# Kernel optimization log

Measured on AMD Instinct MI355X. Metric: run time of the kernel, lower is better.

Reference implementation:

```python
import jax, jax.numpy as jnp
import numpy as np

B, S, I = 16, 512, 64
D, H, L, F = 512, 8, 6, 2048
MAX_REL = 32
EPS = 1e-5


def setup_inputs() -> dict:
    key = jax.random.key(0)
    ks = jax.random.split(key, 16)
    sc = 0.02
    inp = {
        "x": jax.random.normal(ks[0], (B, S, I), dtype=jnp.float32),
        "in_W": jax.random.normal(ks[1], (I, D), dtype=jnp.float32) * sc,
        "in_b": jnp.zeros((D,), jnp.float32),
        "rel_emb": jax.random.normal(ks[2], (2 * MAX_REL + 1, D), dtype=jnp.float32) * sc,
        "qkvo_W": jax.random.normal(ks[3], (L, 4, D, D), dtype=jnp.float32) * sc,
        "qkvo_b": jnp.zeros((L, 4, D), jnp.float32),
        "ln_g": jnp.ones((L, 2, D), jnp.float32),
        "ln_b": jnp.zeros((L, 2, D), jnp.float32),
        "ff_W1": jax.random.normal(ks[4], (L, D, F), dtype=jnp.float32) * sc,
        "ff_b1": jnp.zeros((L, F), jnp.float32),
        "ff_W2": jax.random.normal(ks[5], (L, F, D), dtype=jnp.float32) * sc,
        "ff_b2": jnp.zeros((L, D), jnp.float32),
        "out_W": jax.random.normal(ks[6], (D, 1), dtype=jnp.float32) * sc,
        "out_b": jnp.zeros((1,), jnp.float32),
    }
    return inp


def _layernorm(x, g, b):
    mu = jnp.mean(x, axis=-1, keepdims=True)
    var = jnp.mean((x - mu) ** 2, axis=-1, keepdims=True)
    return (x - mu) * jax.lax.rsqrt(var + EPS) * g + b


def reference(x, in_W, in_b, rel_emb, qkvo_W, qkvo_b, ln_g, ln_b, ff_W1, ff_b1, ff_W2, ff_b2, out_W, out_b):
    b, s, _ = x.shape
    dk = D // H
    h = x @ in_W + in_b  # (B,S,D)
    # relative positional encoding: mean over query axis of gathered embeddings
    pos = jnp.arange(s)
    rel = jnp.clip(pos[:, None] - pos[None, :], -MAX_REL, MAX_REL) + MAX_REL  # (S,S)
    rp = rel_emb[rel]  # (S,S,D)
    h = h + rp.mean(axis=0)[None]  # broadcast over batch

    def layer(h, p):
        Wqkvo, bqkvo, g, bl, W1, b1, W2, b2 = p
        def proj(i):
            return (h @ Wqkvo[i] + bqkvo[i]).reshape(b, s, H, dk).transpose(0, 2, 1, 3)
        q, k, v = proj(0), proj(1), proj(2)  # (B,H,S,dk)
        scores = jnp.einsum("bhqd,bhkd->bhqk", q, k) / jnp.sqrt(jnp.float32(dk))
        attn = jax.nn.softmax(scores, axis=-1)
        ctx = jnp.einsum("bhqk,bhkd->bhqd", attn, v)
        ctx = ctx.transpose(0, 2, 1, 3).reshape(b, s, D)
        ao = ctx @ Wqkvo[3] + bqkvo[3]
        h1 = _layernorm(h + ao, g[0], bl[0])
        ff = jax.nn.relu(h1 @ W1 + b1) @ W2 + b2
        h2 = _layernorm(h1 + ff, g[1], bl[1])
        return h2, None

    h, _ = jax.lax.scan(layer, h, (qkvo_W, qkvo_b, ln_g, ln_b, ff_W1, ff_b1, ff_W2, ff_b2))
    out = h @ out_W + out_b  # (B,S,1)
    return out
```

## Files before the change

kernel.cpp:

```cpp
#include <hip/hip_runtime.h>
#include <math.h>

#define B 16
#define S 512
#define IN 64
#define D 512
#define H 8
#define DK 64
#define L 6
#define F 2048
#define BS (B*S)
#define EPS 1e-5f

typedef short short8 __attribute__((ext_vector_type(8)));
typedef short short4v __attribute__((ext_vector_type(4)));
typedef float floatx4 __attribute__((ext_vector_type(4)));

static __device__ inline short f2bf(float x) {
    unsigned u = __float_as_uint(x);
    unsigned r = (u + 0x7fffu + ((u >> 16) & 1u)) >> 16;
    return (short)r;
}
static __device__ inline float bf2f(short s) {
    return __uint_as_float(((unsigned)(unsigned short)s) << 16);
}

__global__ __launch_bounds__(256) void pe_kernel(const float* __restrict__ rel_emb,
                                                 float* __restrict__ pe) {
    int k = blockIdx.x;
    int d = threadIdx.x;
    float acc0 = 0.f, acc1 = 0.f;
    for (int r = 0; r < 65; ++r) {
        float w;
        if (r == 0)       w = (float)max(0, k - 31);
        else if (r == 64) w = (float)max(0, S - (k + 32));
        else {
            int qpos = k + r - 32;
            w = (qpos >= 0 && qpos < S) ? 1.f : 0.f;
        }
        acc0 += w * rel_emb[r * D + d];
        acc1 += w * rel_emb[r * D + d + 256];
    }
    pe[k * D + d]       = acc0 * (1.f / (float)S);
    pe[k * D + d + 256] = acc1 * (1.f / (float)S);
}

__global__ __launch_bounds__(256) void wtrans_kernel(const float* __restrict__ src,
                                                     short* __restrict__ dst,
                                                     int K, int N) {
    __shared__ float Ls[32][33];
    const int z = blockIdx.z, kb = blockIdx.y, nb = blockIdx.x;
    const int tx = threadIdx.x & 31, ty = threadIdx.x >> 5;
    src += (size_t)z * K * N;
    dst += (size_t)z * K * N;
#pragma unroll
    for (int i = 0; i < 4; ++i)
        Ls[ty + i * 8][tx] = src[(size_t)(kb * 32 + ty + i * 8) * N + nb * 32 + tx];
    __syncthreads();
#pragma unroll
    for (int i = 0; i < 4; ++i) {
        int n = nb * 32 + ty + i * 8;
        dst[(size_t)n * K + kb * 32 + tx] = f2bf(Ls[tx][ty + i * 8]);
    }
}

__global__ __launch_bounds__(256) void cvt_kernel(const float* __restrict__ in,
                                                  short* __restrict__ out) {
    int i = (blockIdx.x * 256 + threadIdx.x) * 4;
    float4 v = *(const float4*)(in + i);
    short4v o;
    o.x = f2bf(v.x); o.y = f2bf(v.y); o.z = f2bf(v.z); o.w = f2bf(v.w);
    *(short4v*)(out + i) = o;
}

__global__ __launch_bounds__(256) void vtrans_kernel(const short* __restrict__ v,
                                                     short* __restrict__ vt) {
    __shared__ short Ls[64 * 72];
    const int bh = blockIdx.y, jt = blockIdx.x * 64;
    const int t = threadIdx.x;
    const int r = t >> 2, cg = t & 3;
    *(short8*)&Ls[r * 72 + cg * 8] =
        *(const short8*)(v + ((size_t)bh * S + jt + r) * DK + cg * 8);
    *(short8*)&Ls[r * 72 + 32 + cg * 8] =
        *(const short8*)(v + ((size_t)bh * S + jt + r) * DK + 32 + cg * 8);
    __syncthreads();
    const int d = t >> 2, sg = t & 3;
    short tmp[16];
#pragma unroll
    for (int i = 0; i < 16; ++i) tmp[i] = Ls[(sg * 16 + i) * 72 + d];
    short* dst = vt + ((size_t)bh * DK + d) * S + jt + sg * 16;
    *(short8*)(dst)     = *(short8*)&tmp[0];
    *(short8*)(dst + 8) = *(short8*)&tmp[8];
}

#define GLL(SRC, DST) __builtin_amdgcn_global_load_lds( \
    (const __attribute__((address_space(1))) void*)(SRC), \
    (__attribute__((address_space(3))) void*)(DST), 16, 0, 0)

#define SWAIT4 __builtin_amdgcn_s_waitcnt(0x0F74)
#define SWAIT0 __builtin_amdgcn_s_waitcnt(0x0F70)

#define KITER(CUR_A, CUR_B, NXT_A, NXT_B, I)                              \
  {                                                                       \
    if ((I) + 1 < niter) SWAIT4; else SWAIT0;                             \
    __builtin_amdgcn_s_barrier();                                         \
    const int kn_ = ((I) + 2) << 5;                                       \
    if (kn_ < K) {                                                        \
      GLL(Ag0 + kn_, NXT_A + so0); GLL(Ag1 + kn_, NXT_A + so1);           \
      GLL(Bg0 + kn_, NXT_B + so0); GLL(Bg1 + kn_, NXT_B + so1);           \
    }                                                                     \
    short8 af_[4], bf_[4];                                                \
    _Pragma("unroll")                                                     \
    for (int mt = 0; mt < 4; ++mt) {                                      \
      af_[mt] = *(const short8*)&CUR_A[((wm * 4 + mt) * 64 + slot) * 8];  \
      bf_[mt] = *(const short8*)&CUR_B[((wn * 4 + mt) * 64 + slot) * 8];  \
    }                                                                     \
    _Pragma("unroll")                                                     \
    for (int mt = 0; mt < 4; ++mt)                                        \
      _Pragma("unroll")                                                   \
      for (int nt = 0; nt < 4; ++nt)                                      \
        acc[mt][nt] = __builtin_amdgcn_mfma_f32_16x16x32_bf16(            \
            af_[mt], bf_[nt], acc[mt][nt], 0, 0, 0);                      \
  }

__global__ __launch_bounds__(256) void mfma_gemm(
    const short* __restrict__ A, const short* __restrict__ Bt,
    const float* __restrict__ bias, short* __restrict__ Cb,
    float* __restrict__ Cf, int M, int N, int K, int lda, int ldb, int mode,
    const float* __restrict__ pe, long az, long wz, long bz, long cz)
{
    __shared__ short As0[4096], As1[4096], As2[4096];
    __shared__ short Bs0[4096], Bs1[4096], Bs2[4096];

    const int z = blockIdx.z;
    const short* Az = A  + (size_t)z * az;
    const short* Bz = Bt + (size_t)z * wz;

    const int t = threadIdx.x;
    const int w = t >> 6, lane = t & 63;
    const int wm = w >> 1, wn = w & 1;
    const int ln15 = lane & 15, lq = lane >> 4;
    const int bm = blockIdx.y, bn = blockIdx.x;

    const int ml = lane >> 2;
    const int kb = ((lane & 3) - (ml >> 1)) & 3;
    const short* Ag0 = Az + (size_t)(bm * 128 + w * 16 + ml)       * lda + kb * 8;
    const short* Ag1 = Az + (size_t)(bm * 128 + (w + 4) * 16 + ml) * lda + kb * 8;
    const short* Bg0 = Bz + (size_t)(bn * 128 + w * 16 + ml)       * ldb + kb * 8;
    const short* Bg1 = Bz + (size_t)(bn * 128 + (w + 4) * 16 + ml) * ldb + kb * 8;
    const int so0 = w * 512, so1 = (w + 4) * 512;

    floatx4 acc[4][4] = {};
    const int slot = ln15 * 4 + ((lq + (ln15 >> 1)) & 3);
    const int niter = K >> 5;

    GLL(Ag0, As0 + so0); GLL(Ag1, As0 + so1);
    GLL(Bg0, Bs0 + so0); GLL(Bg1, Bs0 + so1);
    if (niter > 1) {
        GLL(Ag0 + 32, As1 + so0); GLL(Ag1 + 32, As1 + so1);
        GLL(Bg0 + 32, Bs1 + so0); GLL(Bg1 + 32, Bs1 + so1);
    }

    int i = 0;
    for (; i + 3 <= niter; i += 3) {
        KITER(As0, Bs0, As2, Bs2, i);
        KITER(As1, Bs1, As0, Bs0, i + 1);
        KITER(As2, Bs2, As1, Bs1, i + 2);
    }
    if (i < niter)     KITER(As0, Bs0, As2, Bs2, i);
    if (i + 1 < niter) KITER(As1, Bs1, As0, Bs0, i + 1);

    short* Cbz = Cb + (size_t)z * cz;
    float* Cfz = Cf + (size_t)z * cz;
    const float* bb = bias + (size_t)z * bz;
#pragma unroll
    for (int mt = 0; mt < 4; ++mt) {
#pragma unroll
        for (int nt = 0; nt < 4; ++nt) {
            const int col = bn * 128 + wn * 64 + nt * 16 + ln15;
            const int row0 = bm * 128 + wm * 64 + mt * 16 + lq * 4;
            const float bc = (mode == 4) ? 0.f : bb[col];
#pragma unroll
            for (int reg = 0; reg < 4; ++reg) {
                const int r = row0 + reg;
                float v = acc[mt][nt][reg] + bc;
                if (mode == 4) {
                    Cfz[(size_t)r * N + col] = v;
                } else if (mode == 3) {
                    const int bi = r >> 9, si = r & (S - 1);
                    const int hh = col >> 6, dd = col & 63;
                    Cbz[(((size_t)(bi * H + hh) * S + si) * DK + dd)] = f2bf(v);
                } else {
                    if (mode == 1) v = fmaxf(v, 0.f);
                    else if (mode == 2) v += pe[(size_t)(r & (S - 1)) * D + col];
                    Cb[(size_t)r * N + col] = f2bf(v);
                }
            }
        }
    }
}

__global__ __launch_bounds__(256) void attn_mfma(
    const short* __restrict__ qg, const short* __restrict__ kg,
    const short* __restrict__ vtg, short* __restrict__ ctx)
{
    __shared__ short Ks[64 * 72];
    __shared__ short Vs[64 * 72];
    __shared__ short Ps[4][16 * 72];

    const int t = threadIdx.x;
    const int w = t >> 6, lane = t & 63;
    const int ln15 = lane & 15, lq = lane >> 4;
    const int bh = blockIdx.y, bi = bh >> 3, hh = bh & 7;
    const int qbase = blockIdx.x * 64 + w * 16;

    short8 qf0, qf1;
    {
        const short* qrow = qg + ((size_t)bh * S + qbase + ln15) * DK;
        qf0 = *(const short8*)(qrow + lq * 8);
        qf1 = *(const short8*)(qrow + 32 + lq * 8);
    }
    floatx4 o[4] = {};
    float mrow[4] = {-1e30f, -1e30f, -1e30f, -1e30f};
    float lrow[4] = {};

    const int sr = t >> 2, scg = t & 3;
    const short* kbase = kg  + (size_t)bh * S * DK;
    const short* vtb   = vtg + (size_t)bh * DK * S;

    for (int jt = 0; jt < S; jt += 64) {
        __syncthreads();
        *(short8*)&Ks[sr * 72 + scg * 8] =
            *(const short8*)(kbase + (size_t)(jt + sr) * DK + scg * 8);
        *(short8*)&Ks[sr * 72 + 32 + scg * 8] =
            *(const short8*)(kbase + (size_t)(jt + sr) * DK + 32 + scg * 8);
        *(short8*)&Vs[sr * 72 + scg * 8] =
            *(const short8*)(vtb + (size_t)sr * S + jt + scg * 8);
        *(short8*)&Vs[sr * 72 + 32 + scg * 8] =
            *(const short8*)(vtb + (size_t)sr * S + jt + 32 + scg * 8);
        __syncthreads();

        floatx4 sc[4];
#pragma unroll
        for (int nt = 0; nt < 4; ++nt) {
            floatx4 s4 = {};
            short8 kf0 = *(const short8*)&Ks[(nt * 16 + ln15) * 72 + lq * 8];
            short8 kf1 = *(const short8*)&Ks[(nt * 16 + ln15) * 72 + 32 + lq * 8];
            s4 = __builtin_amdgcn_mfma_f32_16x16x32_bf16(qf0, kf0, s4, 0, 0, 0);
            s4 = __builtin_amdgcn_mfma_f32_16x16x32_bf16(qf1, kf1, s4, 0, 0, 0);
#pragma unroll
            for (int r = 0; r < 4; ++r) s4[r] *= 0.125f;
            sc[nt] = s4;
        }

        float rmax[4];
#pragma unroll
        for (int r = 0; r < 4; ++r)
            rmax[r] = fmaxf(fmaxf(sc[0][r], sc[1][r]), fmaxf(sc[2][r], sc[3][r]));
#pragma unroll
        for (int off = 1; off < 16; off <<= 1)
#pragma unroll
            for (int r = 0; r < 4; ++r)
                rmax[r] = fmaxf(rmax[r], __shfl_xor(rmax[r], off));

        float mnew[4], alpha[4], psum[4];
#pragma unroll
        for (int r = 0; r < 4; ++r) {
            mnew[r]  = fmaxf(mrow[r], rmax[r]);
            alpha[r] = __expf(mrow[r] - mnew[r]);
            psum[r]  = 0.f;
        }
#pragma unroll
        for (int nt = 0; nt < 4; ++nt)
#pragma unroll
            for (int r = 0; r < 4; ++r) {
                float p = __expf(sc[nt][r] - mnew[r]);
                psum[r] += p;
                Ps[w][(lq * 4 + r) * 72 + nt * 16 + ln15] = f2bf(p);
            }
#pragma unroll
        for (int off = 1; off < 16; off <<= 1)
#pragma unroll
            for (int r = 0; r < 4; ++r)
                psum[r] += __shfl_xor(psum[r], off);
#pragma unroll
        for (int r = 0; r < 4; ++r) {
            lrow[r] = lrow[r] * alpha[r] + psum[r];
            mrow[r] = mnew[r];
        }
#pragma unroll
        for (int dv = 0; dv < 4; ++dv)
#pragma unroll
            for (int r = 0; r < 4; ++r)
                o[dv][r] *= alpha[r];

        short8 pf0 = *(const short8*)&Ps[w][ln15 * 72 + lq * 8];
        short8 pf1 = *(const short8*)&Ps[w][ln15 * 72 + 32 + lq * 8];
#pragma unroll
        for (int dv = 0; dv < 4; ++dv) {
            short8 vf0 = *(const short8*)&Vs[(dv * 16 + ln15) * 72 + lq * 8];
            short8 vf1 = *(const short8*)&Vs[(dv * 16 + ln15) * 72 + 32 + lq * 8];
            o[dv] = __builtin_amdgcn_mfma_f32_16x16x32_bf16(pf0, vf0, o[dv], 0, 0, 0);
            o[dv] = __builtin_amdgcn_mfma_f32_16x16x32_bf16(pf1, vf1, o[dv], 0, 0, 0);
        }
    }

    float inv[4];
#pragma unroll
    for (int r = 0; r < 4; ++r) inv[r] = 1.f / lrow[r];
#pragma unroll
    for (int dv = 0; dv < 4; ++dv)
#pragma unroll
        for (int r = 0; r < 4; ++r) {
            const int s = qbase + lq * 4 + r;
            const int col = hh * DK + dv * 16 + ln15;
            ctx[((size_t)bi * S + s) * D + col] = f2bf(o[dv][r] * inv[r]);
        }
}

__global__ __launch_bounds__(128) void ln_res_kernel(
    const short* __restrict__ a, const float* __restrict__ p0,
    const float* __restrict__ p1, const float* __restrict__ eb,
    const float* __restrict__ g, const float* __restrict__ beta,
    short* __restrict__ outb)
{
    const int row = blockIdx.x;
    const int t = threadIdx.x;
    const size_t off = (size_t)row * D + t * 4;
    const short4v xa = *(const short4v*)(a + off);
    const float4 q0 = *(const float4*)(p0 + off);
    const float4 q1 = *(const float4*)(p1 + off);
    const float4 bb2 = *(const float4*)(eb + t * 4);
    float x0 = bf2f(xa.x) + q0.x + q1.x + bb2.x;
    float x1 = bf2f(xa.y) + q0.y + q1.y + bb2.y;
    float x2 = bf2f(xa.z) + q0.z + q1.z + bb2.z;
    float x3 = bf2f(xa.w) + q0.w + q1.w + bb2.w;
    float s  = x0 + x1 + x2 + x3;
    float s2 = x0 * x0 + x1 * x1 + x2 * x2 + x3 * x3;
#pragma unroll
    for (int o = 32; o > 0; o >>= 1) {
        s  += __shfl_down(s, o);
        s2 += __shfl_down(s2, o);
    }
    __shared__ float red[2][2];
    const int wave = t >> 6;
    if ((t & 63) == 0) { red[wave][0] = s; red[wave][1] = s2; }
    __syncthreads();
    s  = red[0][0] + red[1][0];
    s2 = red[0][1] + red[1][1];
    const float mu  = s * (1.f / (float)D);
    const float var = s2 * (1.f / (float)D) - mu * mu;
    const float r   = rsqrtf(var + EPS);
    const float4 gg = *(const float4*)(g    + t * 4);
    const float4 bb = *(const float4*)(beta + t * 4);
    short4v ob;
    ob.x = f2bf((x0 - mu) * r * gg.x + bb.x);
    ob.y = f2bf((x1 - mu) * r * gg.y + bb.y);
    ob.z = f2bf((x2 - mu) * r * gg.z + bb.z);
    ob.w = f2bf((x3 - mu) * r * gg.w + bb.w);
    *(short4v*)(outb + off) = ob;
}

__global__ __launch_bounds__(256) void out_kernel(
    const short* __restrict__ h, const float* __restrict__ ow,
    const float* __restrict__ ob, float* __restrict__ out)
{
    const int wave = threadIdx.x >> 6;
    const int lane = threadIdx.x & 63;
    const int row  = blockIdx.x * 4 + wave;
    const short* hp = h + (size_t)row * D;
    float s = 0.f;
#pragma unroll
    for (int u = 0; u < 8; ++u) {
        int d = lane + u * 64;
        s += bf2f(hp[d]) * ow[d];
    }
#pragma unroll
    for (int o = 32; o > 0; o >>= 1) s += __shfl_down(s, o);
    if (lane == 0) out[row] = s + ob[0];
}

extern "C" void kernel_launch(void* const* d_in, const int* in_sizes, int n_in,
                              void* d_out, int out_size, void* d_ws, size_t ws_size,
                              hipStream_t stream) {
    const float* x       = (const float*)d_in[0];
    const float* in_W    = (const float*)d_in[1];
    const float* in_b    = (const float*)d_in[2];
    const float* rel_emb = (const float*)d_in[3];
    const float* qkvo_W  = (const float*)d_in[4];
    const float* qkvo_b  = (const float*)d_in[5];
    const float* ln_g    = (const float*)d_in[6];
    const float* ln_bb   = (const float*)d_in[7];
    const float* ff_W1   = (const float*)d_in[8];
    const float* ff_b1   = (const float*)d_in[9];
    const float* ff_W2   = (const float*)d_in[10];
    const float* ff_b2   = (const float*)d_in[11];
    const float* out_W   = (const float*)d_in[12];
    const float* out_b   = (const float*)d_in[13];
    float* out = (float*)d_out;

    const size_t HSZ = (size_t)BS * D;
    float* pe     = (float*)d_ws;
    float* part0  = pe + (size_t)S * D;
    float* part1  = part0 + HSZ;
    short* h_bf   = (short*)(part1 + HSZ);
    short* h1_bf  = h_bf  + HSZ;
    short* qkv_bf = h1_bf + HSZ;
    short* xb     = qkv_bf + 4 * HSZ;
    short* wt_qkvo = xb + (size_t)BS * IN;
    short* wt_ff1  = wt_qkvo + (size_t)L * 4 * D * D;
    short* wt_ff2  = wt_ff1  + (size_t)L * D * F;
    short* wt_in   = wt_ff2  + (size_t)L * F * D;

    const size_t CZ = (size_t)B * H * S * DK;
    short* qb = qkv_bf;
    short* kb = qkv_bf + CZ;
    short* vb = qkv_bf + 2 * CZ;
    short* vt = qkv_bf + 3 * CZ;
    short* ctx_bf = vb;
    short* ff1_bf = qkv_bf;

    dim3 blk(256);

    pe_kernel<<<dim3(S), blk, 0, stream>>>(rel_emb, pe);
    cvt_kernel<<<dim3(BS * IN / 1024), blk, 0, stream>>>(x, xb);
    wtrans_kernel<<<dim3(D / 32, IN / 32, 1), blk, 0, stream>>>(in_W, wt_in, IN, D);
    wtrans_kernel<<<dim3(D / 32, D / 32, 4 * L), blk, 0, stream>>>(qkvo_W, wt_qkvo, D, D);
    wtrans_kernel<<<dim3(F / 32, D / 32, L), blk, 0, stream>>>(ff_W1, wt_ff1, D, F);
    wtrans_kernel<<<dim3(D / 32, F / 32, L), blk, 0, stream>>>(ff_W2, wt_ff2, F, D);

    mfma_gemm<<<dim3(D / 128, BS / 128, 1), blk, 0, stream>>>(
        xb, wt_in, in_b, h_bf, nullptr, BS, D, IN, IN, IN, 2, pe, 0, 0, 0, 0);

    for (int l = 0; l < L; ++l) {
        const float* bl = qkvo_b + (size_t)l * 4 * D;
        mfma_gemm<<<dim3(D / 128, BS / 128, 3), blk, 0, stream>>>(
            h_bf, wt_qkvo + (size_t)l * 4 * D * D, bl, qkv_bf, nullptr,
            BS, D, D, D, D, 3, nullptr, 0, (long)D * D, (long)D, (long)CZ);
        vtrans_kernel<<<dim3(S / 64, B * H), blk, 0, stream>>>(vb, vt);
        attn_mfma<<<dim3(S / 64, B * H), blk, 0, stream>>>(qb, kb, vt, ctx_bf);
        mfma_gemm<<<dim3(D / 128, BS / 128, 2), blk, 0, stream>>>(
            ctx_bf, wt_qkvo + (size_t)(l * 4 + 3) * D * D, nullptr, nullptr, part0,
            BS, D, 256, D, D, 4, nullptr, 256, 256, 0, (long)HSZ);
        ln_res_kernel<<<dim3(BS), dim3(128), 0, stream>>>(
            h_bf, part0, part1, bl + 3 * D,
            ln_g + (size_t)l * 2 * D, ln_bb + (size_t)l * 2 * D, h1_bf);
        mfma_gemm<<<dim3(F / 128, BS / 128, 1), blk, 0, stream>>>(
            h1_bf, wt_ff1 + (size_t)l * D * F, ff_b1 + (size_t)l * F, ff1_bf, nullptr,
            BS, F, D, D, D, 1, nullptr, 0, 0, 0, 0);
        mfma_gemm<<<dim3(D / 128, BS / 128, 2), blk, 0, stream>>>(
            ff1_bf, wt_ff2 + (size_t)l * F * D, nullptr, nullptr, part0,
            BS, D, 1024, F, F, 4, nullptr, 1024, 1024, 0, (long)HSZ);
        ln_res_kernel<<<dim3(BS), dim3(128), 0, stream>>>(
            h1_bf, part0, part1, ff_b2 + (size_t)l * D,
            ln_g + (size_t)l * 2 * D + D, ln_bb + (size_t)l * 2 * D + D, h_bf);
    }

    out_kernel<<<dim3(BS / 4), blk, 0, stream>>>(h_bf, out_W, out_b, out);
}
```

Baseline: 1.267 ms.

## Replace split-K fp32 partials with 128x64 tile GEMM and fuse V transpose

Two narrow N=512 GEMMs used split-K over two z-slices writing fp32 partials that layernorm then summed. They now use a new 128x64-tile kernel over the full K, adding bias and writing bf16 output directly. This doubles the block count without split-K and cuts fp32 partial traffic. The V projection is written transposed straight from the QKV GEMM epilogue, removing the separate vtrans kernel. The cost is strided scattered stores for V and rounding the residual branch to bf16 before layernorm.

After: 1.206 ms. 1.05x faster.

```diff
diff --git a/kernel.cpp b/kernel.cpp
--- a/kernel.cpp
+++ b/kernel.cpp
@@ -73,31 +73,12 @@
     *(short4v*)(out + i) = o;
 }
 
-__global__ __launch_bounds__(256) void vtrans_kernel(const short* __restrict__ v,
-                                                     short* __restrict__ vt) {
-    __shared__ short Ls[64 * 72];
-    const int bh = blockIdx.y, jt = blockIdx.x * 64;
-    const int t = threadIdx.x;
-    const int r = t >> 2, cg = t & 3;
-    *(short8*)&Ls[r * 72 + cg * 8] =
-        *(const short8*)(v + ((size_t)bh * S + jt + r) * DK + cg * 8);
-    *(short8*)&Ls[r * 72 + 32 + cg * 8] =
-        *(const short8*)(v + ((size_t)bh * S + jt + r) * DK + 32 + cg * 8);
-    __syncthreads();
-    const int d = t >> 2, sg = t & 3;
-    short tmp[16];
-#pragma unroll
-    for (int i = 0; i < 16; ++i) tmp[i] = Ls[(sg * 16 + i) * 72 + d];
-    short* dst = vt + ((size_t)bh * DK + d) * S + jt + sg * 16;
-    *(short8*)(dst)     = *(short8*)&tmp[0];
-    *(short8*)(dst + 8) = *(short8*)&tmp[8];
-}
-
 #define GLL(SRC, DST) __builtin_amdgcn_global_load_lds( \
     (const __attribute__((address_space(1))) void*)(SRC), \
     (__attribute__((address_space(3))) void*)(DST), 16, 0, 0)
 
 #define SWAIT4 __builtin_amdgcn_s_waitcnt(0x0F74)
+#define SWAIT3 __builtin_amdgcn_s_waitcnt(0x0F73)
 #define SWAIT0 __builtin_amdgcn_s_waitcnt(0x0F70)
 
 #define KITER(CUR_A, CUR_B, NXT_A, NXT_B, I)                              \
@@ -126,14 +107,13 @@
 __global__ __launch_bounds__(256) void mfma_gemm(
     const short* __restrict__ A, const short* __restrict__ Bt,
     const float* __restrict__ bias, short* __restrict__ Cb,
-    float* __restrict__ Cf, int M, int N, int K, int lda, int ldb, int mode,
-    const float* __restrict__ pe, long az, long wz, long bz, long cz)
+    int M, int N, int K, int lda, int ldb, int mode,
+    const float* __restrict__ pe, long wz, long bz, long cz)
 {
     __shared__ short As0[4096], As1[4096], As2[4096];
     __shared__ short Bs0[4096], Bs1[4096], Bs2[4096];
 
     const int z = blockIdx.z;
-    const short* Az = A  + (size_t)z * az;
     const short* Bz = Bt + (size_t)z * wz;
 
     const int t = threadIdx.x;
@@ -144,8 +124,8 @@
 
     const int ml = lane >> 2;
     const int kb = ((lane & 3) - (ml >> 1)) & 3;
-    const short* Ag0 = Az + (size_t)(bm * 128 + w * 16 + ml)       * lda + kb * 8;
-    const short* Ag1 = Az + (size_t)(bm * 128 + (w + 4) * 16 + ml) * lda + kb * 8;
+    const short* Ag0 = A  + (size_t)(bm * 128 + w * 16 + ml)       * lda + kb * 8;
+    const short* Ag1 = A  + (size_t)(bm * 128 + (w + 4) * 16 + ml) * lda + kb * 8;
     const short* Bg0 = Bz + (size_t)(bn * 128 + w * 16 + ml)       * ldb + kb * 8;
     const short* Bg1 = Bz + (size_t)(bn * 128 + (w + 4) * 16 + ml) * ldb + kb * 8;
     const int so0 = w * 512, so1 = (w + 4) * 512;
@@ -171,7 +151,6 @@
     if (i + 1 < niter) KITER(As1, Bs1, As0, Bs0, i + 1);
 
     short* Cbz = Cb + (size_t)z * cz;
-    float* Cfz = Cf + (size_t)z * cz;
     const float* bb = bias + (size_t)z * bz;
 #pragma unroll
     for (int mt = 0; mt < 4; ++mt) {
@@ -179,22 +158,102 @@
         for (int nt = 0; nt < 4; ++nt) {
             const int col = bn * 128 + wn * 64 + nt * 16 + ln15;
             const int row0 = bm * 128 + wm * 64 + mt * 16 + lq * 4;
-            const float bc = (mode == 4) ? 0.f : bb[col];
+            const float bc = bb[col];
 #pragma unroll
             for (int reg = 0; reg < 4; ++reg) {
                 const int r = row0 + reg;
                 float v = acc[mt][nt][reg] + bc;
-                if (mode == 4) {
-                    Cfz[(size_t)r * N + col] = v;
-                } else if (mode == 3) {
+                if (mode == 3) {
                     const int bi = r >> 9, si = r & (S - 1);
                     const int hh = col >> 6, dd = col & 63;
-                    Cbz[(((size_t)(bi * H + hh) * S + si) * DK + dd)] = f2bf(v);
+                    if (z == 2)
+                        Cbz[(((size_t)(bi * H + hh) * DK + dd) * S + si)] = f2bf(v);
+                    else
+                        Cbz[(((size_t)(bi * H + hh) * S + si) * DK + dd)] = f2bf(v);
                 } else {
                     if (mode == 1) v = fmaxf(v, 0.f);
                     else if (mode == 2) v += pe[(size_t)(r & (S - 1)) * D + col];
                     Cb[(size_t)r * N + col] = f2bf(v);
                 }
+            }
+        }
+    }
+}
+
+#define KITER64(CUR_A, CUR_B, NXT_A, NXT_B, I)                            \
+  {                                                                       \
+    if ((I) + 1 < niter) SWAIT3; else SWAIT0;                             \
+    __builtin_amdgcn_s_barrier();                                         \
+    const int kn_ = ((I) + 2) << 5;                                       \
+    if (kn_ < K) {                                                        \
+      GLL(Ag0 + kn_, NXT_A + so0); GLL(Ag1 + kn_, NXT_A + so1);           \
+      GLL(Bg0 + kn_, NXT_B + sob);                                        \
+    }                                                                     \
+    short8 af_[2], bf_[4];                                                \
+    _Pragma("unroll")                                                     \
+    for (int mt = 0; mt < 2; ++mt)                                        \
+      af_[mt] = *(const short8*)&CUR_A[((w * 2 + mt) * 64 + slot) * 8];   \
+    _Pragma("unroll")                                                     \
+    for (int nt = 0; nt < 4; ++nt)                                        \
+      bf_[nt] = *(const short8*)&CUR_B[(nt * 64 + slot) * 8];             \
+    _Pragma("unroll")                                                     \
+    for (int mt = 0; mt < 2; ++mt)                                        \
+      _Pragma("unroll")                                                   \
+      for (int nt = 0; nt < 4; ++nt)                                      \
+        acc[mt][nt] = __builtin_amdgcn_mfma_f32_16x16x32_bf16(            \
+            af_[mt], bf_[nt], acc[mt][nt], 0, 0, 0);                      \
+  }
+
+__global__ __launch_bounds__(256) void mfma_gemm_n64(
+    const short* __restrict__ A, const short* __restrict__ Bt,
+    const float* __restrict__ bias, short* __restrict__ Cb,
+    int M, int N, int K, int lda, int ldb, int mode)
+{
+    __shared__ short As0[4096], As1[4096], As2[4096];
+    __shared__ short Bs0[2048], Bs1[2048], Bs2[2048];
+
+    const int t = threadIdx.x;
+    const int w = t >> 6, lane = t & 63;
+    const int ln15 = lane & 15, lq = lane >> 4;
+    const int bm = blockIdx.y, bn = blockIdx.x;
+
+    const int ml = lane >> 2;
+    const int kb = ((lane & 3) - (ml >> 1)) & 3;
+    const short* Ag0 = A  + (size_t)(bm * 128 + w * 16 + ml)       * lda + kb * 8;
+    const short* Ag1 = A  + (size_t)(bm * 128 + (w + 4) * 16 + ml) * lda + kb * 8;
+    const short* Bg0 = Bt + (size_t)(bn * 64 + w * 16 + ml)        * ldb + kb * 8;
+    const int so0 = w * 512, so1 = (w + 4) * 512, sob = w * 512;
+
+    floatx4 acc[2][4] = {};
+    const int slot = ln15 * 4 + ((lq + (ln15 >> 1)) & 3);
+    const int niter = K >> 5;
+
+    GLL(Ag0, As0 + so0); GLL(Ag1, As0 + so1); GLL(Bg0, Bs0 + sob);
+    if (niter > 1) {
+        GLL(Ag0 + 32, As1 + so0); GLL(Ag1 + 32, As1 + so1); GLL(Bg0 + 32, Bs1 + sob);
+    }
+
+    int i = 0;
+    for (; i + 3 <= niter; i += 3) {
+        KITER64(As0, Bs0, As2, Bs2, i);
+        KITER64(As1, Bs1, As0, Bs0, i + 1);
+        KITER64(As2, Bs2, As1, Bs1, i + 2);
+    }
+    if (i < niter)     KITER64(As0, Bs0, As2, Bs2, i);
+    if (i + 1 < niter) KITER64(As1, Bs1, As0, Bs0, i + 1);
+
+#pragma unroll
+    for (int mt = 0; mt < 2; ++mt) {
+#pragma unroll
+        for (int nt = 0; nt < 4; ++nt) {
+            const int col = bn * 64 + nt * 16 + ln15;
+            const int row0 = bm * 128 + w * 32 + mt * 16 + lq * 4;
+            const float bc = bias[col];
+#pragma unroll
+            for (int reg = 0; reg < 4; ++reg) {
+                float v = acc[mt][nt][reg] + bc;
+                if (mode == 1) v = fmaxf(v, 0.f);
+                Cb[(size_t)(row0 + reg) * N + col] = f2bf(v);
             }
         }
     }
@@ -318,9 +377,8 @@
         }
 }
 
-__global__ __launch_bounds__(128) void ln_res_kernel(
-    const short* __restrict__ a, const float* __restrict__ p0,
-    const float* __restrict__ p1, const float* __restrict__ eb,
+__global__ __launch_bounds__(128) void ln_kernel(
+    const short* __restrict__ a, const short* __restrict__ bres,
     const float* __restrict__ g, const float* __restrict__ beta,
     short* __restrict__ outb)
 {
@@ -328,13 +386,9 @@
     const int t = threadIdx.x;
     const size_t off = (size_t)row * D + t * 4;
     const short4v xa = *(const short4v*)(a + off);
-    const float4 q0 = *(const float4*)(p0 + off);
-    const float4 q1 = *(const float4*)(p1 + off);
-    const float4 bb2 = *(const float4*)(eb + t * 4);
-    float x0 = bf2f(xa.x) + q0.x + q1.x + bb2.x;
-    float x1 = bf2f(xa.y) + q0.y + q1.y + bb2.y;
-    float x2 = bf2f(xa.z) + q0.z + q1.z + bb2.z;
-    float x3 = bf2f(xa.w) + q0.w + q1.w + bb2.w;
+    const short4v xb = *(const short4v*)(bres + off);
+    float x0 = bf2f(xa.x) + bf2f(xb.x), x1 = bf2f(xa.y) + bf2f(xb.y);
+    float x2 = bf2f(xa.z) + bf2f(xb.z), x3 = bf2f(xa.w) + bf2f(xb.w);
     float s  = x0 + x1 + x2 + x3;
     float s2 = x0 * x0 + x1 * x1 + x2 * x2 + x3 * x3;
 #pragma unroll
@@ -401,11 +455,10 @@
 
     const size_t HSZ = (size_t)BS * D;
     float* pe     = (float*)d_ws;
-    float* part0  = pe + (size_t)S * D;
-    float* part1  = part0 + HSZ;
-    short* h_bf   = (short*)(part1 + HSZ);
+    short* h_bf   = (short*)(pe + (size_t)S * D);
     short* h1_bf  = h_bf  + HSZ;
-    short* qkv_bf = h1_bf + HSZ;
+    short* tmp_bf = h1_bf + HSZ;
+    short* qkv_bf = tmp_bf + HSZ;
     short* xb     = qkv_bf + 4 * HSZ;
     short* wt_qkvo = xb + (size_t)BS * IN;
     short* wt_ff1  = wt_qkvo + (size_t)L * 4 * D * D;
@@ -415,9 +468,8 @@
     const size_t CZ = (size_t)B * H * S * DK;
     short* qb = qkv_bf;
     short* kb = qkv_bf + CZ;
-    short* vb = qkv_bf + 2 * CZ;
-    short* vt = qkv_bf + 3 * CZ;
-    short* ctx_bf = vb;
+    short* vt = qkv_bf + 2 * CZ;
+    short* ctx_bf = qkv_bf + 3 * CZ;
     short* ff1_bf = qkv_bf;
 
     dim3 blk(256);
@@ -430,30 +482,28 @@
     wtrans_kernel<<<dim3(D / 32, F / 32, L), blk, 0, stream>>>(ff_W2, wt_ff2, F, D);
 
     mfma_gemm<<<dim3(D / 128, BS / 128, 1), blk, 0, stream>>>(
-        xb, wt_in, in_b, h_bf, nullptr, BS, D, IN, IN, IN, 2, pe, 0, 0, 0, 0);
+        xb, wt_in, in_b, h_bf, BS, D, IN, IN, IN, 2, pe, 0, 0, 0);
 
     for (int l = 0; l < L; ++l) {
         const float* bl = qkvo_b + (size_t)l * 4 * D;
         mfma_gemm<<<dim3(D / 128, BS / 128, 3), blk, 0, stream>>>(
-            h_bf, wt_qkvo + (size_t)l * 4 * D * D, bl, qkv_bf, nullptr,
-            BS, D, D, D, D, 3, nullptr, 0, (long)D * D, (long)D, (long)CZ);
-        vtrans_kernel<<<dim3(S / 64, B * H), blk, 0, stream>>>(vb, vt);
+            h_bf, wt_qkvo + (size_t)l * 4 * D * D, bl, qkv_bf,
+            BS, D, D, D, D, 3, nullptr, (long)D * D, (long)D, (long)CZ);
         attn_mfma<<<dim3(S / 64, B * H), blk, 0, stream>>>(qb, kb, vt, ctx_bf);
-        mfma_gemm<<<dim3(D / 128, BS / 128, 2), blk, 0, stream>>>(
-            ctx_bf, wt_qkvo + (size_t)(l * 4 + 3) * D * D, nullptr, nullptr, part0,
-            BS, D, 256, D, D, 4, nullptr, 256, 256, 0, (long)HSZ);
-        ln_res_kernel<<<dim3(BS), dim3(128), 0, stream>>>(
-            h_bf, part0, part1, bl + 3 * D,
-            ln_g + (size_t)l * 2 * D, ln_bb + (size_t)l * 2 * D, h1_bf);
+        mfma_gemm_n64<<<dim3(D / 64, BS / 128), blk, 0, stream>>>(
+            ctx_bf, wt_qkvo + (size_t)(l * 4 + 3) * D * D, bl + 3 * D, tmp_bf,
+            BS, D, D, D, D, 0);
+        ln_kernel<<<dim3(BS), dim3(128), 0, stream>>>(
+            h_bf, tmp_bf, ln_g + (size_t)l * 2 * D, ln_bb + (size_t)l * 2 * D, h1_bf);
         mfma_gemm<<<dim3(F / 128, BS / 128, 1), blk, 0, stream>>>(
-            h1_bf, wt_ff1 + (size_t)l * D * F, ff_b1 + (size_t)l * F, ff1_bf, nullptr,
-            BS, F, D, D, D, 1, nullptr, 0, 0, 0, 0);
-        mfma_gemm<<<dim3(D / 128, BS / 128, 2), blk, 0, stream>>>(
-            ff1_bf, wt_ff2 + (size_t)l * F * D, nullptr, nullptr, part0,
-            BS, D, 1024, F, F, 4, nullptr, 1024, 1024, 0, (long)HSZ);
-        ln_res_kernel<<<dim3(BS), dim3(128), 0, stream>>>(
-            h1_bf, part0, part1, ff_b2 + (size_t)l * D,
-            ln_g + (size_t)l * 2 * D + D, ln_bb + (size_t)l * 2 * D + D, h_bf);
+            h1_bf, wt_ff1 + (size_t)l * D * F, ff_b1 + (size_t)l * F, ff1_bf,
+            BS, F, D, D, D, 1, nullptr, 0, 0, 0);
+        mfma_gemm_n64<<<dim3(D / 64, BS / 128), blk, 0, stream>>>(
+            ff1_bf, wt_ff2 + (size_t)l * F * D, ff_b2 + (size_t)l * D, tmp_bf,
+            BS, D, F, F, F, 0);
+        ln_kernel<<<dim3(BS), dim3(128), 0, stream>>>(
+            h1_bf, tmp_bf, ln_g + (size_t)l * 2 * D + D, ln_bb + (size_t)l * 2 * D + D,
+            h_bf);
     }
 
     out_kernel<<<dim3(BS / 4), blk, 0, stream>>>(h_bf, out_W, out_b, out);
```
